# Performance work log

Measured on AMD Instinct MI355X. Metric: run time of the kernel, lower is better.

Reference implementation:

```python
import jax, jax.numpy as jnp
import numpy as np


def _local_similar(q, k, kH, kW):
    # q, k: [B, C, H, W] -> scores [B, H, W, kH*kW]
    # Matches similar_forward: zero-padded kH x kW neighborhood dot products.
    B, C, H, W = q.shape
    pH, pW = kH // 2, kW // 2
    kp = jnp.pad(k, ((0, 0), (0, 0), (pH, pH), (pW, pW)))
    scores = [
        jnp.einsum('bchw,bchw->bhw', q, kp[:, :, dh:dh + H, dw:dw + W])
        for dh in range(kH) for dw in range(kW)
    ]
    return jnp.stack(scores, axis=-1)


def _local_weighting(v, w, kH, kW):
    # v: [B, C, H, W], w: [B, H, W, kH*kW] -> out [B, C, H, W]
    # Matches weighting_forward: weighted sum over zero-padded neighborhood.
    B, C, H, W = v.shape
    pH, pW = kH // 2, kW // 2
    vp = jnp.pad(v, ((0, 0), (0, 0), (pH, pH), (pW, pW)))
    out = jnp.zeros_like(v)
    idx = 0
    for dh in range(kH):
        for dw in range(kW):
            out = out + w[..., idx][:, None, :, :] * vp[:, :, dh:dh + H, dw:dw + W]
            idx += 1
    return out


def setup_inputs() -> dict:
    key = jax.random.key(0)
    k1, k2, k3, k4 = jax.random.split(key, 4)
    B, C, H, W = 8, 64, 128, 128
    O = 64  # out_channels
    scale = 1.0 / np.sqrt(C).astype(np.float32)
    x = jax.random.normal(k1, (B, C, H, W), jnp.float32)
    W1 = jax.random.normal(k2, (O, C), jnp.float32) * scale  # conv1 (1x1, no bias)
    W2 = jax.random.normal(k3, (O, C), jnp.float32) * scale  # conv2
    W3 = jax.random.normal(k4, (O, C), jnp.float32) * scale  # conv3
    return {"x": x, "W1": W1, "W2": W2, "W3": W3, "kH": 7, "kW": 7}


def reference(x, W1, W2, W3, kH, kW):
    # 1x1 convs == per-pixel channel matmuls
    q = jnp.einsum('oc,bchw->bohw', W1, x)
    k = jnp.einsum('oc,bchw->bohw', W2, x)
    v = jnp.einsum('oc,bchw->bohw', W3, x)
    scores = _local_similar(q, k, kH, kW)          # [B, H, W, kH*kW]
    w = jax.nn.softmax(scores, axis=-1)
    return _local_weighting(v, w, kH, kW)          # [B, O, H, W]
```

## Files before the change

kernel.cpp:

```cpp
#include <hip/hip_runtime.h>
#include <hip/hip_bf16.h>

#define B_ 8
#define C_ 64
#define H_ 128
#define W_ 128
#define HW_ (H_ * W_)

typedef __attribute__((ext_vector_type(8))) short short8;
typedef __attribute__((ext_vector_type(4))) float float4v;
typedef _Float16 f16x2 __attribute__((ext_vector_type(2)));

static __device__ inline unsigned bfbits(float f) {
    __hip_bfloat16 h = __float2bfloat16(f);
    unsigned short s;
    __builtin_memcpy(&s, &h, 2);
    return (unsigned)s;
}

static __device__ inline float dot2(unsigned a, unsigned b, float c) {
    f16x2 ha, hb;
    __builtin_memcpy(&ha, &a, 4);
    __builtin_memcpy(&hb, &b, 4);
#if __has_builtin(__builtin_amdgcn_fdot2)
    return __builtin_amdgcn_fdot2(ha, hb, c, false);
#else
    return fmaf((float)ha.x, (float)hb.x, fmaf((float)ha.y, (float)hb.y, c));
#endif
}

static __device__ inline float2 up2(unsigned u) {
    f16x2 h;
    __builtin_memcpy(&h, &u, 4);
    return make_float2((float)h.x, (float)h.y);
}

__global__ void repack_w(const float* __restrict__ w1, const float* __restrict__ w2,
                         const float* __restrict__ w3,
                         unsigned short* __restrict__ wBhi, unsigned short* __restrict__ wBlo)
{
    const int i = blockIdx.x * 256 + threadIdx.x;
    if (i >= 12288) return;
    const int j = i & 7, lane = (i >> 3) & 63, ks = (i >> 9) & 1, nt = i >> 10;
    const int o = nt * 16 + (lane & 15);
    const int c = ks * 32 + (lane >> 4) * 8 + j;
    const float* wsel = (o < 64) ? w1 : (o < 128) ? w2 : w3;
    const float w = wsel[(o & 63) * 64 + c];
    const unsigned hb = bfbits(w);
    wBhi[i] = (unsigned short)hb;
    wBlo[i] = (unsigned short)bfbits(w - __uint_as_float(hb << 16));
}

__global__ __launch_bounds__(256, 2) void proj_qkv(
    const float* __restrict__ x,
    const unsigned short* __restrict__ wBhi, const unsigned short* __restrict__ wBlo,
    _Float16* __restrict__ q, _Float16* __restrict__ k, _Float16* __restrict__ v)
{
    const int b = blockIdx.y;
    const int px0 = blockIdx.x * 128;
    const int t = threadIdx.x;
    const int lane = t & 63;
    const int wave_m = (t >> 6) & 1, wave_n = t >> 7;
    const int n = lane & 15, kg = lane >> 4;

    float4v acc[6][4];
    #pragma unroll
    for (int tnt = 0; tnt < 6; ++tnt)
        #pragma unroll
        for (int mt = 0; mt < 4; ++mt)
            acc[tnt][mt] = (float4v){0.f, 0.f, 0.f, 0.f};

    const float* xb = x + (size_t)b * C_ * HW_;
    const int pxl = px0 + wave_m * 64 + n;

    #pragma unroll
    for (int ks = 0; ks < 2; ++ks) {
        short8 ahi[4], alo[4];
        #pragma unroll
        for (int mt = 0; mt < 4; ++mt) {
            #pragma unroll
            for (int j = 0; j < 8; ++j) {
                const int c = ks * 32 + kg * 8 + j;
                const float f = xb[(size_t)c * HW_ + pxl + mt * 16];
                const unsigned hb = bfbits(f);
                ahi[mt][j] = (short)hb;
                alo[mt][j] = (short)bfbits(f - __uint_as_float(hb << 16));
            }
        }
        #pragma unroll
        for (int tnt = 0; tnt < 6; ++tnt) {
            const size_t bidx = (((size_t)(wave_n * 6 + tnt) * 2 + ks) * 64 + lane) * 8;
            short8 bh, bl;
            {
                const uint4 uh = *(const uint4*)(wBhi + bidx);
                const uint4 ul = *(const uint4*)(wBlo + bidx);
                __builtin_memcpy(&bh, &uh, 16);
                __builtin_memcpy(&bl, &ul, 16);
            }
            #pragma unroll
            for (int mt = 0; mt < 4; ++mt) {
                acc[tnt][mt] = __builtin_amdgcn_mfma_f32_16x16x32_bf16(
                    ahi[mt], bh, acc[tnt][mt], 0, 0, 0);
                acc[tnt][mt] = __builtin_amdgcn_mfma_f32_16x16x32_bf16(
                    alo[mt], bh, acc[tnt][mt], 0, 0, 0);
                acc[tnt][mt] = __builtin_amdgcn_mfma_f32_16x16x32_bf16(
                    ahi[mt], bl, acc[tnt][mt], 0, 0, 0);
            }
        }
    }

    #pragma unroll
    for (int tnt = 0; tnt < 6; ++tnt) {
        const int o_base = wave_n * 96 + tnt * 16;
        _Float16* base = (o_base < 64) ? q : (o_base < 128) ? k : v;
        const int chunk = (o_base >> 4) & 3;
        #pragma unroll
        for (int mt = 0; mt < 4; ++mt) {
            const int pxm = px0 + wave_m * 64 + mt * 16 + kg * 4;
            const float4v d = acc[tnt][mt];
            _Float16* p = base + (((size_t)b * 4 + chunk) * HW_ + pxm) * 16 + n;
            #pragma unroll
            for (int r = 0; r < 4; ++r) p[(size_t)r * 16] = (_Float16)d[r];
        }
    }
}

#define HP_ 484
#define PL_ 1944

__global__ __launch_bounds__(256, 2) void local_attn(
    const _Float16* __restrict__ q, const _Float16* __restrict__ k,
    const _Float16* __restrict__ v, float* __restrict__ out)
{
    __shared__ float tile[8 * PL_];
    const int b = blockIdx.z, h0 = blockIdx.y * 16, w0 = blockIdx.x * 16;
    const int t = threadIdx.x;
    const int pw = t & 15, ph = t >> 4;
    const size_t px = (size_t)(h0 + ph) * W_ + (w0 + pw);

    uint4 qv[8];
    #pragma unroll
    for (int c8 = 0; c8 < 8; ++c8)
        qv[c8] = *(const uint4*)(q + (((size_t)b * 4 + (c8 >> 1)) * HW_ + px) * 16 + (c8 & 1) * 8);

    for (int i = t; i < HP_ * 8; i += 256) {
        const int pix = i >> 3, c8 = i & 7;
        const int r = pix / 22, cl = pix - r * 22;
        const int gh = h0 + r - 3, gw = w0 + cl - 3;
        uint4 val = make_uint4(0u, 0u, 0u, 0u);
        if (gh >= 0 && gh < H_ && gw >= 0 && gw < W_)
            val = *(const uint4*)(k + (((size_t)b * 4 + (c8 >> 1)) * HW_ +
                                       (size_t)gh * W_ + gw) * 16 + (c8 & 1) * 8);
        *(uint4*)(tile + c8 * PL_ + pix * 4) = val;
    }
    __syncthreads();

    float sc[49];
    #pragma unroll
    for (int dh = 0; dh < 7; ++dh) {
        #pragma unroll
        for (int dw = 0; dw < 7; ++dw) {
            const int np = ((ph + dh) * 22 + (pw + dw)) * 4;
            float s0 = 0.f, s1 = 0.f, s2 = 0.f, s3 = 0.f;
            #pragma unroll
            for (int p8 = 0; p8 < 8; ++p8) {
                const uint4 u = *(const uint4*)(tile + p8 * PL_ + np);
                s0 = dot2(qv[p8].x, u.x, s0);
                s1 = dot2(qv[p8].y, u.y, s1);
                s2 = dot2(qv[p8].z, u.z, s2);
                s3 = dot2(qv[p8].w, u.w, s3);
            }
            sc[dh * 7 + dw] = (s0 + s1) + (s2 + s3);
        }
    }

    float m = sc[0];
    #pragma unroll
    for (int i = 1; i < 49; ++i) m = fmaxf(m, sc[i]);
    float s = 0.f;
    #pragma unroll
    for (int i = 0; i < 49; ++i) { sc[i] = __expf(sc[i] - m); s += sc[i]; }
    const float inv = 1.f / s;
    #pragma unroll
    for (int i = 0; i < 49; ++i) sc[i] *= inv;

    __syncthreads();

    for (int i = t; i < HP_ * 8; i += 256) {
        const int pix = i >> 3, c8 = i & 7;
        const int r = pix / 22, cl = pix - r * 22;
        const int gh = h0 + r - 3, gw = w0 + cl - 3;
        uint4 val = make_uint4(0u, 0u, 0u, 0u);
        if (gh >= 0 && gh < H_ && gw >= 0 && gw < W_)
            val = *(const uint4*)(v + (((size_t)b * 4 + (c8 >> 1)) * HW_ +
                                       (size_t)gh * W_ + gw) * 16 + (c8 & 1) * 8);
        *(uint4*)(tile + c8 * PL_ + pix * 4) = val;
    }
    __syncthreads();

    #pragma unroll 1
    for (int g = 0; g < 2; ++g) {
        float acc[32];
        #pragma unroll
        for (int c = 0; c < 32; ++c) acc[c] = 0.f;
        #pragma unroll
        for (int dh = 0; dh < 7; ++dh) {
            #pragma unroll
            for (int dw = 0; dw < 7; ++dw) {
                const float wgt = sc[dh * 7 + dw];
                const int np = ((ph + dh) * 22 + (pw + dw)) * 4;
                #pragma unroll
                for (int pp = 0; pp < 4; ++pp) {
                    const uint4 u = *(const uint4*)(tile + (g * 4 + pp) * PL_ + np);
                    const int a = pp * 8;
                    float2 f;
                    f = up2(u.x); acc[a + 0] = fmaf(wgt, f.x, acc[a + 0]);
                                  acc[a + 1] = fmaf(wgt, f.y, acc[a + 1]);
                    f = up2(u.y); acc[a + 2] = fmaf(wgt, f.x, acc[a + 2]);
                                  acc[a + 3] = fmaf(wgt, f.y, acc[a + 3]);
                    f = up2(u.z); acc[a + 4] = fmaf(wgt, f.x, acc[a + 4]);
                                  acc[a + 5] = fmaf(wgt, f.y, acc[a + 5]);
                    f = up2(u.w); acc[a + 6] = fmaf(wgt, f.x, acc[a + 6]);
                                  acc[a + 7] = fmaf(wgt, f.y, acc[a + 7]);
                }
            }
        }
        #pragma unroll
        for (int pp = 0; pp < 4; ++pp) {
            const int p8 = g * 4 + pp;
            const int ch0 = (p8 >> 1) * 16 + (p8 & 1) * 8;
            #pragma unroll
            for (int j = 0; j < 8; ++j)
                out[((size_t)b * 64 + ch0 + j) * HW_ + px] = acc[pp * 8 + j];
        }
    }
}

extern "C" void kernel_launch(void* const* d_in, const int* in_sizes, int n_in,
                              void* d_out, int out_size, void* d_ws, size_t ws_size,
                              hipStream_t stream) {
    const float* x  = (const float*)d_in[0];
    const float* w1 = (const float*)d_in[1];
    const float* w2 = (const float*)d_in[2];
    const float* w3 = (const float*)d_in[3];

    const size_t NE = (size_t)B_ * 4 * HW_ * 16;
    _Float16* q = (_Float16*)d_ws;
    _Float16* k = q + NE;
    _Float16* v = k + NE;
    unsigned short* wBhi = (unsigned short*)(v + NE);
    unsigned short* wBlo = wBhi + 12288;
    float* o = (float*)d_out;

    repack_w<<<dim3(48), 256, 0, stream>>>(w1, w2, w3, wBhi, wBlo);
    proj_qkv<<<dim3(HW_ / 128, B_), 256, 0, stream>>>(x, wBhi, wBlo, q, k, v);
    local_attn<<<dim3(W_ / 16, H_ / 16, B_), 256, 0, stream>>>(q, k, v, o);
}
```

Baseline: 160.3 us.

## Pipeline local attention with direct-to-LDS loads and split proj waves

The local attention kernel now stages K and V halo tiles with global_load_lds in four-channel-group halves. While one half is scored or weighted, the next half is staging, so global loads overlap with LDS compute. Halo tiles are zeroed up front only for border blocks, and the per-thread offsets and bounds checks are computed once. The projection kernel moves to 512 threads, with each wave holding half as many output tiles, to cut accumulator register pressure and add waves. The risk is that the async LDS loads depend on the barriers also waiting for outstanding vector memory operations.

```diff
diff --git a/kernel.cpp b/kernel.cpp
--- a/kernel.cpp
+++ b/kernel.cpp
@@ -33,6 +33,16 @@
     f16x2 h;
     __builtin_memcpy(&h, &u, 4);
     return make_float2((float)h.x, (float)h.y);
+}
+
+static __device__ __attribute__((always_inline)) void glds16(const void* g, void* l) {
+#if __has_builtin(__builtin_amdgcn_global_load_lds)
+    __builtin_amdgcn_global_load_lds(
+        (const __attribute__((address_space(1))) void*)g,
+        (__attribute__((address_space(3))) void*)l, 16, 0, 0);
+#else
+    *(uint4*)l = *(const uint4*)g;
+#endif
 }
 
 __global__ void repack_w(const float* __restrict__ w1, const float* __restrict__ w2,
@@ -51,7 +61,7 @@
     wBlo[i] = (unsigned short)bfbits(w - __uint_as_float(hb << 16));
 }
 
-__global__ __launch_bounds__(256, 2) void proj_qkv(
+__global__ __launch_bounds__(512, 4) void proj_qkv(
     const float* __restrict__ x,
     const unsigned short* __restrict__ wBhi, const unsigned short* __restrict__ wBlo,
     _Float16* __restrict__ q, _Float16* __restrict__ k, _Float16* __restrict__ v)
@@ -60,12 +70,13 @@
     const int px0 = blockIdx.x * 128;
     const int t = threadIdx.x;
     const int lane = t & 63;
-    const int wave_m = (t >> 6) & 1, wave_n = t >> 7;
+    const int wave = t >> 6;
+    const int wave_m = wave & 1, wave_n = wave >> 1;
     const int n = lane & 15, kg = lane >> 4;
 
-    float4v acc[6][4];
-    #pragma unroll
-    for (int tnt = 0; tnt < 6; ++tnt)
+    float4v acc[3][4];
+    #pragma unroll
+    for (int tnt = 0; tnt < 3; ++tnt)
         #pragma unroll
         for (int mt = 0; mt < 4; ++mt)
             acc[tnt][mt] = (float4v){0.f, 0.f, 0.f, 0.f};
@@ -88,8 +99,9 @@
             }
         }
         #pragma unroll
-        for (int tnt = 0; tnt < 6; ++tnt) {
-            const size_t bidx = (((size_t)(wave_n * 6 + tnt) * 2 + ks) * 64 + lane) * 8;
+        for (int tnt = 0; tnt < 3; ++tnt) {
+            const int gnt = wave_n * 3 + tnt;
+            const size_t bidx = (((size_t)gnt * 2 + ks) * 64 + lane) * 8;
             short8 bh, bl;
             {
                 const uint4 uh = *(const uint4*)(wBhi + bidx);
@@ -110,10 +122,10 @@
     }
 
     #pragma unroll
-    for (int tnt = 0; tnt < 6; ++tnt) {
-        const int o_base = wave_n * 96 + tnt * 16;
-        _Float16* base = (o_base < 64) ? q : (o_base < 128) ? k : v;
-        const int chunk = (o_base >> 4) & 3;
+    for (int tnt = 0; tnt < 3; ++tnt) {
+        const int gnt = wave_n * 3 + tnt;
+        _Float16* base = (gnt < 4) ? q : (gnt < 8) ? k : v;
+        const int chunk = gnt & 3;
         #pragma unroll
         for (int mt = 0; mt < 4; ++mt) {
             const int pxm = px0 + wave_m * 64 + mt * 16 + kg * 4;
@@ -125,54 +137,122 @@
     }
 }
 
-#define HP_ 484
-#define PL_ 1944
+#define PW_ 2048
+
+static __device__ inline void stage_half(const _Float16* __restrict__ src, int b,
+                                         float* tile, int p8base, int wv,
+                                         bool okA, size_t gofsA, bool okB, size_t gofsB)
+{
+    #pragma unroll
+    for (int pp = 0; pp < 4; ++pp) {
+        const int p8 = p8base + pp;
+        const _Float16* gp = src + ((size_t)(b * 4 + (p8 >> 1)) * HW_) * 16 + (p8 & 1) * 8;
+        float* lp = tile + p8 * PW_ + wv * 256;
+        if (okA) glds16(gp + gofsA * 16, lp);
+        if (okB) glds16(gp + gofsB * 16, lp + 1024);
+    }
+}
+
+static __device__ inline void score_half(const float* tp, const uint4* qv,
+                                         float* sc, int ph, int pw)
+{
+    #pragma unroll
+    for (int dh = 0; dh < 7; ++dh) {
+        #pragma unroll
+        for (int dw = 0; dw < 7; ++dw) {
+            const int np = ((ph + dh) * 22 + (pw + dw)) * 4;
+            float s0 = 0.f, s1 = 0.f, s2 = 0.f, s3 = 0.f;
+            #pragma unroll
+            for (int pp = 0; pp < 4; ++pp) {
+                const uint4 u = *(const uint4*)(tp + pp * PW_ + np);
+                s0 = dot2(qv[pp].x, u.x, s0);
+                s1 = dot2(qv[pp].y, u.y, s1);
+                s2 = dot2(qv[pp].z, u.z, s2);
+                s3 = dot2(qv[pp].w, u.w, s3);
+            }
+            sc[dh * 7 + dw] += (s0 + s1) + (s2 + s3);
+        }
+    }
+}
+
+static __device__ inline void weight_half(const float* tp, const float* sc,
+                                          float* outb, size_t px, int ph, int pw)
+{
+    float acc[32];
+    #pragma unroll
+    for (int c = 0; c < 32; ++c) acc[c] = 0.f;
+    #pragma unroll
+    for (int dh = 0; dh < 7; ++dh) {
+        #pragma unroll
+        for (int dw = 0; dw < 7; ++dw) {
+            const float wgt = sc[dh * 7 + dw];
+            const int np = ((ph + dh) * 22 + (pw + dw)) * 4;
+            #pragma unroll
+            for (int pp = 0; pp < 4; ++pp) {
+                const uint4 u = *(const uint4*)(tp + pp * PW_ + np);
+                const int a = pp * 8;
+                float2 f;
+                f = up2(u.x); acc[a + 0] = fmaf(wgt, f.x, acc[a + 0]);
+                              acc[a + 1] = fmaf(wgt, f.y, acc[a + 1]);
+                f = up2(u.y); acc[a + 2] = fmaf(wgt, f.x, acc[a + 2]);
+                              acc[a + 3] = fmaf(wgt, f.y, acc[a + 3]);
+                f = up2(u.z); acc[a + 4] = fmaf(wgt, f.x, acc[a + 4]);
+                              acc[a + 5] = fmaf(wgt, f.y, acc[a + 5]);
+                f = up2(u.w); acc[a + 6] = fmaf(wgt, f.x, acc[a + 6]);
+                              acc[a + 7] = fmaf(wgt, f.y, acc[a + 7]);
+            }
+        }
+    }
+    #pragma unroll
+    for (int pp = 0; pp < 4; ++pp)
+        #pragma unroll
+        for (int j = 0; j < 8; ++j)
+            outb[(size_t)(pp * 8 + j) * HW_ + px] = acc[pp * 8 + j];
+}
 
 __global__ __launch_bounds__(256, 2) void local_attn(
     const _Float16* __restrict__ q, const _Float16* __restrict__ k,
     const _Float16* __restrict__ v, float* __restrict__ out)
 {
-    __shared__ float tile[8 * PL_];
+    __shared__ float tile[8 * PW_];
     const int b = blockIdx.z, h0 = blockIdx.y * 16, w0 = blockIdx.x * 16;
     const int t = threadIdx.x;
-    const int pw = t & 15, ph = t >> 4;
+    const int pw = t & 15, ph = t >> 4, wv = t >> 6;
     const size_t px = (size_t)(h0 + ph) * W_ + (w0 + pw);
 
+    const int pixA = t, pixB = 256 + t;
+    const int rA = pixA / 22, cA = pixA - rA * 22;
+    const int rB = pixB / 22, cB = pixB - rB * 22;
+    const int ghA = h0 + rA - 3, gwA = w0 + cA - 3;
+    const int ghB = h0 + rB - 3, gwB = w0 + cB - 3;
+    const bool okA = (ghA >= 0 && ghA < H_ && gwA >= 0 && gwA < W_);
+    const bool okB = (pixB < 484) && (ghB >= 0 && ghB < H_ && gwB >= 0 && gwB < W_);
+    const size_t gofsA = (size_t)(ghA * W_ + gwA);
+    const size_t gofsB = (size_t)(ghB * W_ + gwB);
+
+    if (h0 == 0 || h0 == H_ - 16 || w0 == 0 || w0 == W_ - 16) {
+        #pragma unroll
+        for (int i = 0; i < 16; ++i)
+            *(uint4*)(tile + (i * 256 + t) * 4) = make_uint4(0u, 0u, 0u, 0u);
+        __syncthreads();
+    }
+
+    stage_half(k, b, tile, 0, wv, okA, gofsA, okB, gofsB);
     uint4 qv[8];
     #pragma unroll
     for (int c8 = 0; c8 < 8; ++c8)
         qv[c8] = *(const uint4*)(q + (((size_t)b * 4 + (c8 >> 1)) * HW_ + px) * 16 + (c8 & 1) * 8);
-
-    for (int i = t; i < HP_ * 8; i += 256) {
-        const int pix = i >> 3, c8 = i & 7;
-        const int r = pix / 22, cl = pix - r * 22;
-        const int gh = h0 + r - 3, gw = w0 + cl - 3;
-        uint4 val = make_uint4(0u, 0u, 0u, 0u);
-        if (gh >= 0 && gh < H_ && gw >= 0 && gw < W_)
-            val = *(const uint4*)(k + (((size_t)b * 4 + (c8 >> 1)) * HW_ +
-                                       (size_t)gh * W_ + gw) * 16 + (c8 & 1) * 8);
-        *(uint4*)(tile + c8 * PL_ + pix * 4) = val;
-    }
-    __syncthreads();
-
+    __syncthreads();
+
+    stage_half(k, b, tile, 4, wv, okA, gofsA, okB, gofsB);
     float sc[49];
     #pragma unroll
-    for (int dh = 0; dh < 7; ++dh) {
-        #pragma unroll
-        for (int dw = 0; dw < 7; ++dw) {
-            const int np = ((ph + dh) * 22 + (pw + dw)) * 4;
-            float s0 = 0.f, s1 = 0.f, s2 = 0.f, s3 = 0.f;
-            #pragma unroll
-            for (int p8 = 0; p8 < 8; ++p8) {
-                const uint4 u = *(const uint4*)(tile + p8 * PL_ + np);
-                s0 = dot2(qv[p8].x, u.x, s0);
-                s1 = dot2(qv[p8].y, u.y, s1);
-                s2 = dot2(qv[p8].z, u.z, s2);
-                s3 = dot2(qv[p8].w, u.w, s3);
-            }
-            sc[dh * 7 + dw] = (s0 + s1) + (s2 + s3);
-        }
-    }
+    for (int i = 0; i < 49; ++i) sc[i] = 0.f;
+    score_half(tile, qv, sc, ph, pw);
+    __syncthreads();
+
+    stage_half(v, b, tile, 0, wv, okA, gofsA, okB, gofsB);
+    score_half(tile + 4 * PW_, qv + 4, sc, ph, pw);
 
     float m = sc[0];
     #pragma unroll
@@ -183,57 +263,12 @@
     const float inv = 1.f / s;
     #pragma unroll
     for (int i = 0; i < 49; ++i) sc[i] *= inv;
-
-    __syncthreads();
-
-    for (int i = t; i < HP_ * 8; i += 256) {
-        const int pix = i >> 3, c8 = i & 7;
-        const int r = pix / 22, cl = pix - r * 22;
-        const int gh = h0 + r - 3, gw = w0 + cl - 3;
-        uint4 val = make_uint4(0u, 0u, 0u, 0u);
-        if (gh >= 0 && gh < H_ && gw >= 0 && gw < W_)
-            val = *(const uint4*)(v + (((size_t)b * 4 + (c8 >> 1)) * HW_ +
-                                       (size_t)gh * W_ + gw) * 16 + (c8 & 1) * 8);
-        *(uint4*)(tile + c8 * PL_ + pix * 4) = val;
-    }
-    __syncthreads();
-
-    #pragma unroll 1
-    for (int g = 0; g < 2; ++g) {
-        float acc[32];
-        #pragma unroll
-        for (int c = 0; c < 32; ++c) acc[c] = 0.f;
-        #pragma unroll
-        for (int dh = 0; dh < 7; ++dh) {
-            #pragma unroll
-            for (int dw = 0; dw < 7; ++dw) {
-                const float wgt = sc[dh * 7 + dw];
-                const int np = ((ph + dh) * 22 + (pw + dw)) * 4;
-                #pragma unroll
-                for (int pp = 0; pp < 4; ++pp) {
-                    const uint4 u = *(const uint4*)(tile + (g * 4 + pp) * PL_ + np);
-                    const int a = pp * 8;
-                    float2 f;
-                    f = up2(u.x); acc[a + 0] = fmaf(wgt, f.x, acc[a + 0]);
-                                  acc[a + 1] = fmaf(wgt, f.y, acc[a + 1]);
-                    f = up2(u.y); acc[a + 2] = fmaf(wgt, f.x, acc[a + 2]);
-                                  acc[a + 3] = fmaf(wgt, f.y, acc[a + 3]);
-                    f = up2(u.z); acc[a + 4] = fmaf(wgt, f.x, acc[a + 4]);
-                                  acc[a + 5] = fmaf(wgt, f.y, acc[a + 5]);
-                    f = up2(u.w); acc[a + 6] = fmaf(wgt, f.x, acc[a + 6]);
-                                  acc[a + 7] = fmaf(wgt, f.y, acc[a + 7]);
-                }
-            }
-        }
-        #pragma unroll
-        for (int pp = 0; pp < 4; ++pp) {
-            const int p8 = g * 4 + pp;
-            const int ch0 = (p8 >> 1) * 16 + (p8 & 1) * 8;
-            #pragma unroll
-            for (int j = 0; j < 8; ++j)
-                out[((size_t)b * 64 + ch0 + j) * HW_ + px] = acc[pp * 8 + j];
-        }
-    }
+    __syncthreads();
+
+    stage_half(v, b, tile, 4, wv, okA, gofsA, okB, gofsB);
+    weight_half(tile, sc, out + (size_t)b * 64 * HW_, px, ph, pw);
+    __syncthreads();
+    weight_half(tile + 4 * PW_, sc, out + ((size_t)b * 64 + 32) * HW_, px, ph, pw);
 }
 
 extern "C" void kernel_launch(void* const* d_in, const int* in_sizes, int n_in,
@@ -253,6 +288,6 @@
     float* o = (float*)d_out;
 
     repack_w<<<dim3(48), 256, 0, stream>>>(w1, w2, w3, wBhi, wBlo);
-    proj_qkv<<<dim3(HW_ / 128, B_), 256, 0, stream>>>(x, wBhi, wBlo, q, k, v);
+    proj_qkv<<<dim3(HW_ / 128, B_), 512, 0, stream>>>(x, wBhi, wBlo, q, k, v);
     local_attn<<<dim3(W_ / 16, H_ / 16, B_), 256, 0, stream>>>(q, k, v, o);
 }
```

New measurement: 315.4 us. 96.7% more time.
